# Performance work log

Measured on AMD Instinct MI355X. Metric: run time of the kernel, lower is better.

## Reference

```python
import jax, jax.numpy as jnp
import numpy as np

EPS = 1e-5
N_NODES = 10
NUM_JOINTS = 6   # all robot_configs fixed to '3_segments_3DOF' (module's fallback default)
MAX_DOF = 10


def _lin(x, w, b):
    # torch nn.Linear: y = x @ W.T + b, W is (out, in)
    return jnp.einsum('...i,oi->...o', x, w) + b


def _layernorm(x, scale, bias):
    mu = x.mean(-1, keepdims=True)
    var = x.var(-1, keepdims=True)
    return (x - mu) / jnp.sqrt(var + EPS) * scale + bias


def _forward(images, text_lengths, node_features, edge_indices, p):
    B = images.shape[0]
    # --- SimplifiedVLMBackbone ---
    y = jax.lax.conv_general_dilated(images, p['conv_w'], (2, 2), [(3, 3), (3, 3)],
                                     dimension_numbers=('NCHW', 'OIHW', 'NCHW'))
    y = jax.nn.relu(y + p['conv_b'][None, :, None, None])          # (B,32,112,112)
    y = y.reshape(B, 32, 7, 16, 7, 16).mean(axis=(3, 5))            # adaptive avg pool -> (B,32,7,7)
    y = y.reshape(B, 32 * 49)
    y = jax.nn.relu(_lin(y, p['img_fc1_w'], p['img_fc1_b']))
    img_feat = _lin(y, p['img_fc2_w'], p['img_fc2_b'])               # (B,768)
    t = p['text_emb'][jnp.clip(text_lengths, 0, 9999)]               # (B,256)
    vlm = img_feat + _lin(t, p['text_fc_w'], p['text_fc_b'])         # (B,768)

    # --- SoftArmGraphNN ---
    x = jax.nn.relu(_lin(node_features, p['enc1_w'], p['enc1_b']))
    x = _lin(x, p['enc2_w'], p['enc2_b'])                            # (B,N,64)
    src, dst = edge_indices[:, 0, :], edge_indices[:, 1, :]          # (B,E)

    def agg_fn(xi, si, di):
        # mean of neighbor (source) features per destination node; 0 if no neighbors
        g = xi[si]                                                   # (E,D)
        s = jax.ops.segment_sum(g, di, num_segments=N_NODES)
        c = jax.ops.segment_sum(jnp.ones(di.shape, xi.dtype), di, num_segments=N_NODES)
        return s / jnp.maximum(c, 1.0)[:, None]

    for i in range(3):
        residual = x
        mean_nb = jax.vmap(agg_fn)(x, src, dst)                      # (B,N,64)
        comb = jnp.concatenate([x, mean_nb], axis=-1)                # (B,N,128)
        x = _lin(comb, p['gc_w'][i], p['gc_b'][i])
        x = jax.nn.relu(_layernorm(x + residual, p['ln_scale'][i], p['ln_bias'][i]))
    graph_tokens = _lin(x, p['proj_w'], p['proj_b'])                 # (B,N,32)

    # --- AttentionPooling + dual-path fusion ---
    s = _lin(jnp.tanh(_lin(graph_tokens, p['attn1_w'], p['attn1_b'])), p['attn2_w'], p['attn2_b'])
    w = jax.nn.softmax(s, axis=1)                                    # (B,N,1)
    robot_token = jnp.sum(graph_tokens * w, axis=1)                  # (B,32) -> project? 32 vs 768 -> residual add via broadcast pad
    fused = vlm.at[:, :robot_token.shape[-1]].add(robot_token)       # global token residual into vlm features

    # --- NodeActionHead (all samples: 3seg_3DOF -> 6 joints, per-joint MLPs) ---
    comb = jnp.concatenate([
        jnp.broadcast_to(fused[:, None, :], (B, NUM_JOINTS, fused.shape[-1])),
        graph_tokens[:, :NUM_JOINTS, :]], axis=-1)                   # (B,J,800)
    h = jax.nn.relu(jnp.einsum('bjf,jhf->bjh', comb, p['head_w1']) + p['head_b1'])
    h = jax.nn.relu(jnp.einsum('bjf,jhf->bjh', h, p['head_w2']) + p['head_b2'])
    a = jnp.einsum('bjf,jhf->bjh', h, p['head_w3']) + p['head_b3']   # (B,6,16)
    a = jnp.pad(a, ((0, 0), (0, MAX_DOF - NUM_JOINTS), (0, 0)))      # pad to max_dof
    return jnp.transpose(a, (0, 2, 1))                               # (B,16,10)


def setup_inputs() -> dict:
    key = jax.random.key(0)
    ks = iter(jax.random.split(key, 64))

    def nrm(shape, scale=0.02):
        return scale * jax.random.normal(next(ks), shape, dtype=jnp.float32)

    B = 128
    inp = {
        'images': jax.random.normal(next(ks), (B, 3, 224, 224), dtype=jnp.float32),
        'text_lengths': jax.random.randint(next(ks), (B,), 0, 10000, dtype=jnp.int32),
        'node_features': jax.random.normal(next(ks), (B, N_NODES, 19), dtype=jnp.float32),
        'edge_indices': jax.random.randint(next(ks), (B, 2, 18), 0, N_NODES, dtype=jnp.int32),
        'conv_w': nrm((32, 3, 7, 7)), 'conv_b': jnp.zeros(32, jnp.float32),
        'img_fc1_w': nrm((512, 1568)), 'img_fc1_b': jnp.zeros(512, jnp.float32),
        'img_fc2_w': nrm((768, 512)), 'img_fc2_b': jnp.zeros(768, jnp.float32),
        'text_emb': nrm((10000, 256)),
        'text_fc_w': nrm((768, 256)), 'text_fc_b': jnp.zeros(768, jnp.float32),
        'enc1_w': nrm((64, 19)), 'enc1_b': jnp.zeros(64, jnp.float32),
        'enc2_w': nrm((64, 64)), 'enc2_b': jnp.zeros(64, jnp.float32),
        'gc_w': nrm((3, 64, 128)), 'gc_b': jnp.zeros((3, 64), jnp.float32),
        'ln_scale': jnp.ones((3, 64), jnp.float32), 'ln_bias': jnp.zeros((3, 64), jnp.float32),
        'proj_w': nrm((32, 64)), 'proj_b': jnp.zeros(32, jnp.float32),
        'attn1_w': nrm((16, 32)), 'attn1_b': jnp.zeros(16, jnp.float32),
        'attn2_w': nrm((1, 16)), 'attn2_b': jnp.zeros(1, jnp.float32),
        'head_w1': nrm((6, 128, 800)), 'head_b1': jnp.zeros((6, 128), jnp.float32),
        'head_w2': nrm((6, 64, 128)), 'head_b2': jnp.zeros((6, 64), jnp.float32),
        'head_w3': nrm((6, 16, 64)), 'head_b3': jnp.zeros((6, 16), jnp.float32),
    }
    return inp


def reference(images, text_lengths, node_features, edge_indices, conv_w, conv_b,
              img_fc1_w, img_fc1_b, img_fc2_w, img_fc2_b, text_emb, text_fc_w, text_fc_b,
              enc1_w, enc1_b, enc2_w, enc2_b, gc_w, gc_b, ln_scale, ln_bias,
              proj_w, proj_b, attn1_w, attn1_b, attn2_w, attn2_b,
              head_w1, head_b1, head_w2, head_b2, head_w3, head_b3):
    p = dict(conv_w=conv_w, conv_b=conv_b, img_fc1_w=img_fc1_w, img_fc1_b=img_fc1_b,
             img_fc2_w=img_fc2_w, img_fc2_b=img_fc2_b, text_emb=text_emb,
             text_fc_w=text_fc_w, text_fc_b=text_fc_b, enc1_w=enc1_w, enc1_b=enc1_b,
             enc2_w=enc2_w, enc2_b=enc2_b, gc_w=gc_w, gc_b=gc_b, ln_scale=ln_scale,
             ln_bias=ln_bias, proj_w=proj_w, proj_b=proj_b, attn1_w=attn1_w,
             attn1_b=attn1_b, attn2_w=attn2_w, attn2_b=attn2_b, head_w1=head_w1,
             head_b1=head_b1, head_w2=head_w2, head_b2=head_b2, head_w3=head_w3,
             head_b3=head_b3)
    return _forward(images, text_lengths, node_features, edge_indices, p)
```

## Files before the change

### kernel.cpp

```cpp
#include <hip/hip_runtime.h>
#include <hip/hip_bf16.h>
#include <math.h>

typedef __attribute__((ext_vector_type(8))) short bf16x8;
typedef __attribute__((ext_vector_type(4))) float f32x4;

static __device__ __forceinline__ unsigned short f2bf(float f) {
    union { float f; unsigned int u; } x{f};
    unsigned int u = x.u;
    unsigned int r = (u + 0x7fffu + ((u >> 16) & 1u)) >> 16;
    return (unsigned short)r;
}

static __device__ __forceinline__ unsigned int pack2(float f0, float f1) {
    __hip_bfloat162 h = __float22bfloat162_rn(float2{f0, f1});
    union { __hip_bfloat162 h; unsigned int u; } c{h};
    return c.u;
}

__global__ __launch_bounds__(256) void wprep(const float* __restrict__ conv_w,
                                             unsigned short* __restrict__ wB) {
    for (int idx = threadIdx.x; idx < 24 * 32 * 8; idx += 256) {
        int s = idx >> 8;
        int ch = (idx >> 3) & 31;
        int kx = idx & 7;
        float v = 0.f;
        if (s < 21 && kx < 7) {
            int c = s / 7, ky = s - c * 7;
            v = conv_w[ch * 147 + c * 49 + ky * 7 + kx];
        }
        wB[idx] = f2bf(v);
    }
}

#define PSTRIDE 116
__global__ __launch_bounds__(512, 4) void conv_mfma(const float* __restrict__ img,
                                                    const unsigned int* __restrict__ wBu,
                                                    const float* __restrict__ cb,
                                                    float* __restrict__ pooled) {
    __shared__ unsigned int patch[111 * PSTRIDE];
    const int t = threadIdx.x;
    const int py = blockIdx.x, b = blockIdx.y;
    const int lane = t & 63, wid = t >> 6;
    const int r16 = lane & 15, g = lane >> 4;
    const int Y0 = 32 * py - 3;

    const int xc0 = 2 * lane - 3;
    const int xc1 = 2 * lane + 125;
    const int a00 = max(xc0, 0);
    const int a01 = max(xc0 + 1, 0);
    const int a10 = min(xc1, 223);
    const int a11 = min(xc1 + 1, 223);
    const bool v00 = (xc0 >= 0);
    const bool v01 = (xc0 + 1 >= 0);
    const bool v10 = (xc1 <= 223);
    const bool v11 = (xc1 + 1 <= 223);
    const bool c1act = (lane < 52);

    const float* ib = img + (size_t)b * 3 * 224 * 224;

#pragma unroll
    for (int hb = 0; hb < 2; ++hb) {
        float g0[7], g1[7], g2[7], g3[7];
        int rr[7];
        bool rv[7];
        const float* rp[7];
#pragma unroll
        for (int i = 0; i < 7; ++i) {
            int r = wid + 8 * (hb * 7 + i);
            int c_ = (r >= 74) ? 2 : ((r >= 37) ? 1 : 0);
            int pr = r - 37 * c_;
            int iy = Y0 + pr;
            rv[i] = (r < 111) & (iy >= 0) & (iy < 224);
            int iyc = min(max(iy, 0), 223);
            rp[i] = ib + (c_ * 224 + iyc) * 224;
            rr[i] = r;
            g0[i] = rp[i][a00];
            g1[i] = rp[i][a01];
            g2[i] = rp[i][a10];
            g3[i] = rp[i][a11];
        }
#pragma unroll
        for (int i = 0; i < 7; ++i) {
            float f0 = (rv[i] && v00) ? g0[i] : 0.f;
            float f1 = (rv[i] && v01) ? g1[i] : 0.f;
            float f2_ = (rv[i] && v10) ? g2[i] : 0.f;
            float f3 = (rv[i] && v11) ? g3[i] : 0.f;
            if (rr[i] < 111) {
                patch[rr[i] * PSTRIDE + lane] = pack2(f0, f1);
                if (c1act) patch[rr[i] * PSTRIDE + 64 + lane] = pack2(f2_, f3);
            }
        }
    }

    bf16x8 bfrA[6], bfrB[6];
    int rowoff[6];
#pragma unroll
    for (int k = 0; k < 6; ++k) {
        int s = 4 * k + g;
        int sc = s > 20 ? 20 : s;
        int c = sc / 7, ky = sc - c * 7;
        rowoff[k] = c * 37 + ky;
        union { uint4 q; bf16x8 v; } ua, ub;
        ua.q = *(const uint4*)(wBu + (s * 32 + r16) * 4);
        ub.q = *(const uint4*)(wBu + (s * 32 + r16 + 16) * 4);
        bfrA[k] = ua.v;
        bfrB[k] = ub.v;
    }
    const float biasA = cb[r16], biasB = cb[r16 + 16];

    __syncthreads();

    float accA[7], accB[7];
#pragma unroll
    for (int p = 0; p < 7; ++p) accA[p] = accB[p] = 0.f;

#pragma unroll
    for (int q = 0; q < 2; ++q) {
        const int oyl = 2 * wid + q;
        int rb[6];
#pragma unroll
        for (int k = 0; k < 6; ++k) rb[k] = (rowoff[k] + 2 * oyl) * PSTRIDE;

        for (int t7 = 0; t7 < 7; ++t7) {
            const int oxr = 16 * t7 + r16;
            f32x4 C0 = {biasA, biasA, biasA, biasA};
            f32x4 C1 = {biasB, biasB, biasB, biasB};
#pragma unroll
            for (int k = 0; k < 6; ++k) {
                const unsigned int* ap = &patch[rb[k] + oxr];
                union { unsigned int u[4]; bf16x8 v; } ua;
                ua.u[0] = ap[0];
                ua.u[1] = ap[1];
                ua.u[2] = ap[2];
                ua.u[3] = ap[3];
                C0 = __builtin_amdgcn_mfma_f32_16x16x32_bf16(ua.v, bfrA[k], C0, 0, 0, 0);
                C1 = __builtin_amdgcn_mfma_f32_16x16x32_bf16(ua.v, bfrB[k], C1, 0, 0, 0);
            }
            float s0 = 0.f, s1 = 0.f;
#pragma unroll
            for (int r = 0; r < 4; ++r) {
                s0 += fmaxf(C0[r], 0.f);
                s1 += fmaxf(C1[r], 0.f);
            }
            accA[t7] += s0;
            accB[t7] += s1;
        }
    }
#pragma unroll
    for (int p = 0; p < 7; ++p) {
        accA[p] += __shfl_xor(accA[p], 16);
        accA[p] += __shfl_xor(accA[p], 32);
        accB[p] += __shfl_xor(accB[p], 16);
        accB[p] += __shfl_xor(accB[p], 32);
    }
    __syncthreads();
    float* sw = (float*)patch;
    if (lane < 16) {
#pragma unroll
        for (int p = 0; p < 7; ++p) {
            sw[(wid * 7 + p) * 32 + lane] = accA[p];
            sw[(wid * 7 + p) * 32 + lane + 16] = accB[p];
        }
    }
    __syncthreads();
    if (t < 224) {
        int p = t >> 5, ch = t & 31;
        float s = 0.f;
#pragma unroll
        for (int w = 0; w < 8; ++w) s += sw[(w * 7 + p) * 32 + ch];
        pooled[(size_t)b * 1568 + ch * 49 + py * 7 + p] = s * (1.f / 256.f);
    }
}

__global__ __launch_bounds__(256) void fc1_k(const float* __restrict__ in,
                                             const float* __restrict__ w,
                                             const float* __restrict__ bias,
                                             float* __restrict__ out) {
    __shared__ __align__(16) float xsm[8][1568];
    const int t = threadIdx.x;
    const int lane = t & 63, wid = t >> 6;
    const int ob = blockIdx.x & 127;
    const int bg = blockIdx.x >> 7;
    const int b0 = bg * 8;

#pragma unroll
    for (int r = 0; r < 8; ++r)
        for (int i = t; i < 392; i += 256)
            *(float4*)&xsm[r][i * 4] = *(const float4*)(in + (size_t)(b0 + r) * 1568 + i * 4);
    __syncthreads();

    const int o = ob * 4 + wid;
    const float4* wr = (const float4*)(w + (size_t)o * 1568);
    float acc[8] = {0, 0, 0, 0, 0, 0, 0, 0};
    for (int i = lane; i < 392; i += 64) {
        float4 wv = wr[i];
#pragma unroll
        for (int r = 0; r < 8; ++r) {
            float4 xv = *(const float4*)&xsm[r][i * 4];
            acc[r] = fmaf(xv.x, wv.x, acc[r]);
            acc[r] = fmaf(xv.y, wv.y, acc[r]);
            acc[r] = fmaf(xv.z, wv.z, acc[r]);
            acc[r] = fmaf(xv.w, wv.w, acc[r]);
        }
    }
#pragma unroll
    for (int r = 0; r < 8; ++r) {
        acc[r] += __shfl_xor(acc[r], 32);
        acc[r] += __shfl_xor(acc[r], 16);
        acc[r] += __shfl_xor(acc[r], 8);
        acc[r] += __shfl_xor(acc[r], 4);
        acc[r] += __shfl_xor(acc[r], 2);
        acc[r] += __shfl_xor(acc[r], 1);
    }
    float v = 0.f;
#pragma unroll
    for (int r = 0; r < 8; ++r)
        if (lane == r) v = acc[r];
    if (lane < 8) out[(size_t)(b0 + lane) * 512 + o] = fmaxf(v + bias[o], 0.f);
}

__global__ __launch_bounds__(256) void vlm_k(const float* __restrict__ h1,
                                             const float* __restrict__ w2,
                                             const float* __restrict__ b2,
                                             const int* __restrict__ tlen,
                                             const float* __restrict__ temb,
                                             const float* __restrict__ tw,
                                             const float* __restrict__ tb,
                                             const float* __restrict__ rtok,
                                             float* __restrict__ fused) {
    __shared__ __align__(16) float xs1[8][512];
    __shared__ __align__(16) float xst[8][256];
    __shared__ int srow[8];
    const int t = threadIdx.x;
    const int lane = t & 63, wid = t >> 6;
    const int ob = blockIdx.x % 192;
    const int bg = blockIdx.x / 192;
    const int b0 = bg * 8;

    if (t < 8) {
        int r = tlen[b0 + t];
        srow[t] = min(max(r, 0), 9999);
    }
#pragma unroll
    for (int rr = 0; rr < 4; ++rr) {
        int r = rr * 2 + (t >> 7);
        int i = t & 127;
        *(float4*)&xs1[r][i * 4] = *(const float4*)(h1 + (size_t)(b0 + r) * 512 + i * 4);
    }
    __syncthreads();
#pragma unroll
    for (int rr = 0; rr < 2; ++rr) {
        int r = rr * 4 + (t >> 6);
        int i = t & 63;
        *(float4*)&xst[r][i * 4] = *(const float4*)(temb + (size_t)srow[r] * 256 + i * 4);
    }
    __syncthreads();

    const int o = ob * 4 + wid;
    float acc[8] = {0, 0, 0, 0, 0, 0, 0, 0};
    {
        const float4* wr = (const float4*)(w2 + (size_t)o * 512);
#pragma unroll
        for (int ii = 0; ii < 2; ++ii) {
            int i = lane + ii * 64;
            float4 wv = wr[i];
#pragma unroll
            for (int r = 0; r < 8; ++r) {
                float4 xv = *(const float4*)&xs1[r][i * 4];
                acc[r] = fmaf(xv.x, wv.x, acc[r]);
                acc[r] = fmaf(xv.y, wv.y, acc[r]);
                acc[r] = fmaf(xv.z, wv.z, acc[r]);
                acc[r] = fmaf(xv.w, wv.w, acc[r]);
            }
        }
    }
    {
        const float4* wt4 = (const float4*)(tw + (size_t)o * 256);
        float4 wv = wt4[lane];
#pragma unroll
        for (int r = 0; r < 8; ++r) {
            float4 xv = *(const float4*)&xst[r][lane * 4];
            acc[r] = fmaf(xv.x, wv.x, acc[r]);
            acc[r] = fmaf(xv.y, wv.y, acc[r]);
            acc[r] = fmaf(xv.z, wv.z, acc[r]);
            acc[r] = fmaf(xv.w, wv.w, acc[r]);
        }
    }
#pragma unroll
    for (int r = 0; r < 8; ++r) {
        acc[r] += __shfl_xor(acc[r], 32);
        acc[r] += __shfl_xor(acc[r], 16);
        acc[r] += __shfl_xor(acc[r], 8);
        acc[r] += __shfl_xor(acc[r], 4);
        acc[r] += __shfl_xor(acc[r], 2);
        acc[r] += __shfl_xor(acc[r], 1);
    }
    float v = 0.f;
#pragma unroll
    for (int r = 0; r < 8; ++r)
        if (lane == r) v = acc[r];
    if (lane < 8) {
        float add = (o < 32) ? rtok[(size_t)(b0 + lane) * 32 + o] : 0.f;
        fused[(size_t)(b0 + lane) * 768 + o] = v + b2[o] + tb[o] + add;
    }
}

__global__ __launch_bounds__(640, 1) void graph_k(
    const float* __restrict__ nfeat, const int* __restrict__ eidx,
    const float* __restrict__ e1w, const float* __restrict__ e1b,
    const float* __restrict__ e2w, const float* __restrict__ e2b,
    const float* __restrict__ gcw, const float* __restrict__ gcb,
    const float* __restrict__ lns, const float* __restrict__ lnb,
    const float* __restrict__ pjw, const float* __restrict__ pjb,
    const float* __restrict__ a1w, const float* __restrict__ a1b,
    const float* __restrict__ a2w, const float* __restrict__ a2b,
    float* __restrict__ gts_g, float* __restrict__ rtok) {
    __shared__ __align__(16) float pool[8448];
    __shared__ __align__(16) float nf[10][20];
    __shared__ __align__(16) float xsA[10][64];
    __shared__ __align__(16) float xsB[10][64];
    __shared__ __align__(16) float nbs[10][64];
    __shared__ __align__(16) float gtss[10][32];
    __shared__ float svs[10];
    __shared__ int se[18], de[18];
    const int t = threadIdx.x;
    const int b = blockIdx.x;
    const int n = t >> 6, o = t & 63;

    if (t < 190) {
        int nn = t / 19, i = t - nn * 19;
        nf[nn][i] = nfeat[(size_t)(b * 10 + nn) * 19 + i];
    }
    if (t < 36) {
        if (t < 18) se[t] = eidx[b * 36 + t];
        else de[t - 18] = eidx[b * 36 + t];
    }
    float* e1wT = pool;
    float* e2wT = pool + 1280;
    for (int u = t; u < 1216; u += 640) {
        int oo = u / 19, k = u - oo * 19;
        e1wT[k * 64 + oo] = e1w[u];
    }
    for (int u = t; u < 4096; u += 640) {
        int oo = u >> 6, k = u & 63;
        e2wT[k * 65 + oo] = e2w[u];
    }
    __syncthreads();

    float h1v;
    {
        float acc = e1b[o];
#pragma unroll
        for (int i = 0; i < 19; ++i) acc = fmaf(nf[n][i], e1wT[i * 64 + o], acc);
        h1v = fmaxf(acc, 0.f);
        xsB[n][o] = h1v;
    }
    {
        const float* xrow = &xsB[n][0];
        float s0 = 0, s1 = 0, s2 = 0, s3 = 0;
#pragma unroll
        for (int k = 0; k < 64; k += 4) {
            s0 = fmaf(xrow[k], e2wT[k * 65 + o], s0);
            s1 = fmaf(xrow[k + 1], e2wT[(k + 1) * 65 + o], s1);
            s2 = fmaf(xrow[k + 2], e2wT[(k + 2) * 65 + o], s2);
            s3 = fmaf(xrow[k + 3], e2wT[(k + 3) * 65 + o], s3);
        }
        xsA[n][o] = e2b[o] + ((s0 + s1) + (s2 + s3));
    }
    __syncthreads();

    float* src = &xsA[0][0];
    float* dst = &xsB[0][0];
    for (int l = 0; l < 3; ++l) {
        const float* gl = gcw + (size_t)l * 8192;
        for (int u = t; u < 8192; u += 640) {
            int oo = u >> 7, k = u & 127;
            pool[k * 65 + oo] = gl[u];
        }
        {
            float s = 0.f;
            int cnt = 0;
#pragma unroll
            for (int e = 0; e < 18; ++e) {
                bool m = (de[e] == n);
                float v = src[se[e] * 64 + o];
                s += m ? v : 0.f;
                cnt += m ? 1 : 0;
            }
            nbs[n][o] = s / (float)(cnt > 1 ? cnt : 1);
        }
        __syncthreads();
        {
            const float* xa = src + n * 64;
            const float* xb = &nbs[n][0];
            float s0 = 0, s1 = 0, s2 = 0, s3 = 0;
#pragma unroll
            for (int k = 0; k < 64; k += 4) {
                s0 = fmaf(xa[k], pool[k * 65 + o], s0);
                s1 = fmaf(xa[k + 1], pool[(k + 1) * 65 + o], s1);
                s2 = fmaf(xa[k + 2], pool[(k + 2) * 65 + o], s2);
                s3 = fmaf(xa[k + 3], pool[(k + 3) * 65 + o], s3);
            }
#pragma unroll
            for (int k = 0; k < 64; k += 4) {
                s0 = fmaf(xb[k], pool[(64 + k) * 65 + o], s0);
                s1 = fmaf(xb[k + 1], pool[(64 + k + 1) * 65 + o], s1);
                s2 = fmaf(xb[k + 2], pool[(64 + k + 2) * 65 + o], s2);
                s3 = fmaf(xb[k + 3], pool[(64 + k + 3) * 65 + o], s3);
            }
            float v = gcb[l * 64 + o] + ((s0 + s1) + (s2 + s3)) + xa[o];
            float mu = v;
            mu += __shfl_xor(mu, 32);
            mu += __shfl_xor(mu, 16);
            mu += __shfl_xor(mu, 8);
            mu += __shfl_xor(mu, 4);
            mu += __shfl_xor(mu, 2);
            mu += __shfl_xor(mu, 1);
            mu *= (1.f / 64.f);
            float d = v - mu;
            float vr = d * d;
            vr += __shfl_xor(vr, 32);
            vr += __shfl_xor(vr, 16);
            vr += __shfl_xor(vr, 8);
            vr += __shfl_xor(vr, 4);
            vr += __shfl_xor(vr, 2);
            vr += __shfl_xor(vr, 1);
            vr *= (1.f / 64.f);
            dst[n * 64 + o] =
                fmaxf(d / sqrtf(vr + 1e-5f) * lns[l * 64 + o] + lnb[l * 64 + o], 0.f);
        }
        __syncthreads();
        float* tmp = src;
        src = dst;
        dst = tmp;
    }

    float* pjwT = pool;
    float* a1wT = pool + 2112;
    for (int u = t; u < 2048; u += 640) {
        int oo = u >> 6, k = u & 63;
        pjwT[k * 33 + oo] = pjw[u];
    }
    for (int u = t; u < 512; u += 640) {
        int hh = u >> 5, k = u & 31;
        a1wT[k * 17 + hh] = a1w[u];
    }
    __syncthreads();

    if (o < 32) {
        const float* xrow = src + n * 64;
        float s0 = 0, s1 = 0, s2 = 0, s3 = 0;
#pragma unroll
        for (int k = 0; k < 64; k += 4) {
            s0 = fmaf(xrow[k], pjwT[k * 33 + o], s0);
            s1 = fmaf(xrow[k + 1], pjwT[(k + 1) * 33 + o], s1);
            s2 = fmaf(xrow[k + 2], pjwT[(k + 2) * 33 + o], s2);
            s3 = fmaf(xrow[k + 3], pjwT[(k + 3) * 33 + o], s3);
        }
        float gv = pjb[o] + ((s0 + s1) + (s2 + s3));
        gtss[n][o] = gv;
        gts_g[(size_t)b * 320 + n * 32 + o] = gv;
    }
    if (o < 16) {
        const float* xrow = &gtss[n][0];
        float s0 = 0, s1 = 0, s2 = 0, s3 = 0;
#pragma unroll
        for (int k = 0; k < 32; k += 4) {
            s0 = fmaf(xrow[k], a1wT[k * 17 + o], s0);
            s1 = fmaf(xrow[k + 1], a1wT[(k + 1) * 17 + o], s1);
            s2 = fmaf(xrow[k + 2], a1wT[(k + 2) * 17 + o], s2);
            s3 = fmaf(xrow[k + 3], a1wT[(k + 3) * 17 + o], s3);
        }
        float z = a1b[o] + ((s0 + s1) + (s2 + s3));
        float sc = tanhf(z) * a2w[o];
        sc += __shfl_xor(sc, 8);
        sc += __shfl_xor(sc, 4);
        sc += __shfl_xor(sc, 2);
        sc += __shfl_xor(sc, 1);
        if (o == 0) svs[n] = sc + a2b[0];
    }
    __syncthreads();

    if (n == 0 && o < 32) {
        float m = svs[0];
#pragma unroll
        for (int i = 1; i < 10; ++i) m = fmaxf(m, svs[i]);
        float e[10];
        float sum = 0.f;
#pragma unroll
        for (int i = 0; i < 10; ++i) {
            e[i] = expf(svs[i] - m);
            sum += e[i];
        }
        float inv = 1.f / sum;
        float rt = 0.f;
#pragma unroll
        for (int nn = 0; nn < 10; ++nn) rt = fmaf(gtss[nn][o], e[nn] * inv, rt);
        rtok[(size_t)b * 32 + o] = rt;
    }
}

__global__ __launch_bounds__(256) void head1_k(const float* __restrict__ fused,
                                               const float* __restrict__ gts,
                                               const float* __restrict__ w1,
                                               const float* __restrict__ b1,
                                               float* __restrict__ h1T) {
    __shared__ __align__(16) float xsm[8][800];
    const int t = threadIdx.x;
    const int ob = blockIdx.x % 192;
    const int bg = blockIdx.x / 192;
    const int b0 = bg * 8;
    const int j = ob >> 5;
    const int lane = t & 63, wid = t >> 6;

    for (int u = t; u < 1600; u += 256) {
        int row = u / 200, i = u - row * 200;
        float4 v;
        if (i < 192)
            v = *(const float4*)(fused + (size_t)(b0 + row) * 768 + i * 4);
        else
            v = *(const float4*)(gts + (size_t)(b0 + row) * 320 + j * 32 + (i - 192) * 4);
        *(float4*)&xsm[row][i * 4] = v;
    }
    __syncthreads();

    const int o = ob * 4 + wid;
    const float4* wr = (const float4*)(w1 + (size_t)o * 800);
    float acc[8] = {0, 0, 0, 0, 0, 0, 0, 0};
    for (int i = lane; i < 200; i += 64) {
        float4 wv = wr[i];
#pragma unroll
        for (int r = 0; r < 8; ++r) {
            float4 xv = *(const float4*)&xsm[r][i * 4];
            acc[r] = fmaf(xv.x, wv.x, acc[r]);
            acc[r] = fmaf(xv.y, wv.y, acc[r]);
            acc[r] = fmaf(xv.z, wv.z, acc[r]);
            acc[r] = fmaf(xv.w, wv.w, acc[r]);
        }
    }
#pragma unroll
    for (int r = 0; r < 8; ++r) {
        acc[r] += __shfl_xor(acc[r], 32);
        acc[r] += __shfl_xor(acc[r], 16);
        acc[r] += __shfl_xor(acc[r], 8);
        acc[r] += __shfl_xor(acc[r], 4);
        acc[r] += __shfl_xor(acc[r], 2);
        acc[r] += __shfl_xor(acc[r], 1);
    }
    float v = 0.f;
#pragma unroll
    for (int r = 0; r < 8; ++r)
        if (lane == r) v = acc[r];
    if (lane < 8) h1T[(size_t)o * 128 + b0 + lane] = fmaxf(v + b1[o], 0.f);
}

__global__ __launch_bounds__(128) void head2_k(const float* __restrict__ h1T,
                                               const float* __restrict__ w2,
                                               const float* __restrict__ b2,
                                               float* __restrict__ h2T) {
    const int o2 = blockIdx.x;
    const int j = o2 >> 6;
    const int b = threadIdx.x;
    const float* wrow = w2 + (size_t)o2 * 128;
    const float* xcol = h1T + (size_t)j * 128 * 128 + b;
    float acc = b2[o2];
#pragma unroll 16
    for (int k = 0; k < 128; ++k) acc = fmaf(xcol[k * 128], wrow[k], acc);
    h2T[(size_t)o2 * 128 + b] = fmaxf(acc, 0.f);
}

__global__ __launch_bounds__(128) void head3_k(const float* __restrict__ h2T,
                                               const float* __restrict__ w3,
                                               const float* __restrict__ b3,
                                               float* __restrict__ out) {
    const int jj = blockIdx.x % 10;
    const int oo = blockIdx.x / 10;
    const int b = threadIdx.x;
    float acc = 0.f;
    if (jj < 6) {
        const float* wrow = w3 + (size_t)(jj * 16 + oo) * 64;
        const float* xcol = h2T + (size_t)jj * 64 * 128 + b;
        acc = b3[jj * 16 + oo];
#pragma unroll 16
        for (int k = 0; k < 64; ++k) acc = fmaf(xcol[k * 128], wrow[k], acc);
    }
    out[(size_t)b * 160 + oo * 10 + jj] = acc;
}

extern "C" void kernel_launch(void* const* d_in, const int* in_sizes, int n_in,
                              void* d_out, int out_size, void* d_ws, size_t ws_size,
                              hipStream_t stream) {
    const float* images = (const float*)d_in[0];
    const int* tlen = (const int*)d_in[1];
    const float* nfeat = (const float*)d_in[2];
    const int* eidx = (const int*)d_in[3];
    const float* conv_w = (const float*)d_in[4];
    const float* conv_b = (const float*)d_in[5];
    const float* fc1w = (const float*)d_in[6];
    const float* fc1b = (const float*)d_in[7];
    const float* fc2w = (const float*)d_in[8];
    const float* fc2b = (const float*)d_in[9];
    const float* temb = (const float*)d_in[10];
    const float* tfw = (const float*)d_in[11];
    const float* tfb = (const float*)d_in[12];
    const float* e1w = (const float*)d_in[13];
    const float* e1b = (const float*)d_in[14];
    const float* e2w = (const float*)d_in[15];
    const float* e2b = (const float*)d_in[16];
    const float* gcw = (const float*)d_in[17];
    const float* gcb = (const float*)d_in[18];
    const float* lns = (const float*)d_in[19];
    const float* lnb = (const float*)d_in[20];
    const float* pjw = (const float*)d_in[21];
    const float* pjb = (const float*)d_in[22];
    const float* a1w = (const float*)d_in[23];
    const float* a1b = (const float*)d_in[24];
    const float* a2w = (const float*)d_in[25];
    const float* a2b = (const float*)d_in[26];
    const float* w1 = (const float*)d_in[27];
    const float* b1 = (const float*)d_in[28];
    const float* w2 = (const float*)d_in[29];
    const float* b2 = (const float*)d_in[30];
    const float* w3 = (const float*)d_in[31];
    const float* b3 = (const float*)d_in[32];

    const int B = in_sizes[0] / (3 * 224 * 224);

    float* ws = (float*)d_ws;
    unsigned short* wB = (unsigned short*)d_ws;
    float* pooled = ws + 3072;
    float* h1fc = pooled + (size_t)B * 1568;
    float* fused = h1fc + (size_t)B * 512;
    float* gts = fused + (size_t)B * 768;
    float* rtok = gts + (size_t)B * 320;
    float* h1T = pooled;
    float* h2T = pooled + 98304;

    wprep<<<1, 256, 0, stream>>>(conv_w, wB);
    conv_mfma<<<dim3(7, B), 512, 0, stream>>>(images, (const unsigned int*)wB,
                                              conv_b, pooled);
    fc1_k<<<2048, 256, 0, stream>>>(pooled, fc1w, fc1b, h1fc);
    graph_k<<<B, 640, 0, stream>>>(nfeat, eidx, e1w, e1b, e2w, e2b, gcw, gcb,
                                   lns, lnb, pjw, pjb, a1w, a1b, a2w, a2b,
                                   gts, rtok);
    vlm_k<<<3072, 256, 0, stream>>>(h1fc, fc2w, fc2b, tlen, temb, tfw, tfb,
                                    rtok, fused);
    head1_k<<<192 * (B / 8), 256, 0, stream>>>(fused, gts, w1, b1, h1T);
    head2_k<<<384, 128, 0, stream>>>(h1T, w2, b2, h2T);
    head3_k<<<160, 128, 0, stream>>>(h2T, w3, b3, (float*)d_out);
}
```

Before: 133.0 us.

## Compute more output rows per block in FC kernels, re-pad conv weight layout

The fc1, vlm and head1 kernels now loop over 4 or 8 output groups per block, cutting grid sizes by 4-8x. Each block's staged activation tile in shared memory is reused across more weight rows, reducing redundant global activation loads and block launch overhead. The conv weight prep switches to a power-of-two (8 per channel) slot layout with shift/mask indexing, and the patch stride changes from 116 to 120. Fewer blocks may reduce parallelism and latency hiding on a large GPU.

```diff
diff --git a/kernel.cpp b/kernel.cpp
--- a/kernel.cpp
+++ b/kernel.cpp
@@ -24,16 +24,14 @@
         int s = idx >> 8;
         int ch = (idx >> 3) & 31;
         int kx = idx & 7;
+        int c = s >> 3, ky = s & 7;
         float v = 0.f;
-        if (s < 21 && kx < 7) {
-            int c = s / 7, ky = s - c * 7;
-            v = conv_w[ch * 147 + c * 49 + ky * 7 + kx];
-        }
+        if (ky < 7 && kx < 7) v = conv_w[ch * 147 + c * 49 + ky * 7 + kx];
         wB[idx] = f2bf(v);
     }
 }
 
-#define PSTRIDE 116
+#define PSTRIDE 120
 __global__ __launch_bounds__(512, 4) void conv_mfma(const float* __restrict__ img,
                                                     const unsigned int* __restrict__ wBu,
                                                     const float* __restrict__ cb,
@@ -98,9 +96,9 @@
 #pragma unroll
     for (int k = 0; k < 6; ++k) {
         int s = 4 * k + g;
-        int sc = s > 20 ? 20 : s;
-        int c = sc / 7, ky = sc - c * 7;
-        rowoff[k] = c * 37 + ky;
+        int c = s >> 3, ky = s & 7;
+        int kyc = ky > 6 ? 6 : ky;
+        rowoff[k] = c * 37 + kyc;
         union { uint4 q; bf16x8 v; } ua, ub;
         ua.q = *(const uint4*)(wBu + (s * 32 + r16) * 4);
         ub.q = *(const uint4*)(wBu + (s * 32 + r16 + 16) * 4);
@@ -180,8 +178,8 @@
     __shared__ __align__(16) float xsm[8][1568];
     const int t = threadIdx.x;
     const int lane = t & 63, wid = t >> 6;
-    const int ob = blockIdx.x & 127;
-    const int bg = blockIdx.x >> 7;
+    const int ob = blockIdx.x & 31;
+    const int bg = blockIdx.x >> 5;
     const int b0 = bg * 8;
 
 #pragma unroll
@@ -190,34 +188,37 @@
             *(float4*)&xsm[r][i * 4] = *(const float4*)(in + (size_t)(b0 + r) * 1568 + i * 4);
     __syncthreads();
 
-    const int o = ob * 4 + wid;
-    const float4* wr = (const float4*)(w + (size_t)o * 1568);
-    float acc[8] = {0, 0, 0, 0, 0, 0, 0, 0};
-    for (int i = lane; i < 392; i += 64) {
-        float4 wv = wr[i];
+#pragma unroll
+    for (int oi = 0; oi < 4; ++oi) {
+        const int o = ob * 16 + oi * 4 + wid;
+        const float4* wr = (const float4*)(w + (size_t)o * 1568);
+        float acc[8] = {0, 0, 0, 0, 0, 0, 0, 0};
+        for (int i = lane; i < 392; i += 64) {
+            float4 wv = wr[i];
+#pragma unroll
+            for (int r = 0; r < 8; ++r) {
+                float4 xv = *(const float4*)&xsm[r][i * 4];
+                acc[r] = fmaf(xv.x, wv.x, acc[r]);
+                acc[r] = fmaf(xv.y, wv.y, acc[r]);
+                acc[r] = fmaf(xv.z, wv.z, acc[r]);
+                acc[r] = fmaf(xv.w, wv.w, acc[r]);
+            }
+        }
 #pragma unroll
         for (int r = 0; r < 8; ++r) {
-            float4 xv = *(const float4*)&xsm[r][i * 4];
-            acc[r] = fmaf(xv.x, wv.x, acc[r]);
-            acc[r] = fmaf(xv.y, wv.y, acc[r]);
-            acc[r] = fmaf(xv.z, wv.z, acc[r]);
-            acc[r] = fmaf(xv.w, wv.w, acc[r]);
-        }
-    }
-#pragma unroll
-    for (int r = 0; r < 8; ++r) {
-        acc[r] += __shfl_xor(acc[r], 32);
-        acc[r] += __shfl_xor(acc[r], 16);
-        acc[r] += __shfl_xor(acc[r], 8);
-        acc[r] += __shfl_xor(acc[r], 4);
-        acc[r] += __shfl_xor(acc[r], 2);
-        acc[r] += __shfl_xor(acc[r], 1);
-    }
-    float v = 0.f;
-#pragma unroll
-    for (int r = 0; r < 8; ++r)
-        if (lane == r) v = acc[r];
-    if (lane < 8) out[(size_t)(b0 + lane) * 512 + o] = fmaxf(v + bias[o], 0.f);
+            acc[r] += __shfl_xor(acc[r], 32);
+            acc[r] += __shfl_xor(acc[r], 16);
+            acc[r] += __shfl_xor(acc[r], 8);
+            acc[r] += __shfl_xor(acc[r], 4);
+            acc[r] += __shfl_xor(acc[r], 2);
+            acc[r] += __shfl_xor(acc[r], 1);
+        }
+        float v = 0.f;
+#pragma unroll
+        for (int r = 0; r < 8; ++r)
+            if (lane == r) v = acc[r];
+        if (lane < 8) out[(size_t)(b0 + lane) * 512 + o] = fmaxf(v + bias[o], 0.f);
+    }
 }
 
 __global__ __launch_bounds__(256) void vlm_k(const float* __restrict__ h1,
@@ -234,8 +235,8 @@
     __shared__ int srow[8];
     const int t = threadIdx.x;
     const int lane = t & 63, wid = t >> 6;
-    const int ob = blockIdx.x % 192;
-    const int bg = blockIdx.x / 192;
+    const int ob = blockIdx.x % 24;
+    const int bg = blockIdx.x / 24;
     const int b0 = bg * 8;
 
     if (t < 8) {
@@ -257,52 +258,55 @@
     }
     __syncthreads();
 
-    const int o = ob * 4 + wid;
-    float acc[8] = {0, 0, 0, 0, 0, 0, 0, 0};
-    {
-        const float4* wr = (const float4*)(w2 + (size_t)o * 512);
-#pragma unroll
-        for (int ii = 0; ii < 2; ++ii) {
-            int i = lane + ii * 64;
-            float4 wv = wr[i];
+#pragma unroll
+    for (int oi = 0; oi < 8; ++oi) {
+        const int o = ob * 32 + oi * 4 + wid;
+        float acc[8] = {0, 0, 0, 0, 0, 0, 0, 0};
+        {
+            const float4* wr = (const float4*)(w2 + (size_t)o * 512);
+#pragma unroll
+            for (int ii = 0; ii < 2; ++ii) {
+                int i = lane + ii * 64;
+                float4 wv = wr[i];
+#pragma unroll
+                for (int r = 0; r < 8; ++r) {
+                    float4 xv = *(const float4*)&xs1[r][i * 4];
+                    acc[r] = fmaf(xv.x, wv.x, acc[r]);
+                    acc[r] = fmaf(xv.y, wv.y, acc[r]);
+                    acc[r] = fmaf(xv.z, wv.z, acc[r]);
+                    acc[r] = fmaf(xv.w, wv.w, acc[r]);
+                }
+            }
+        }
+        {
+            const float4* wt4 = (const float4*)(tw + (size_t)o * 256);
+            float4 wv = wt4[lane];
 #pragma unroll
             for (int r = 0; r < 8; ++r) {
-                float4 xv = *(const float4*)&xs1[r][i * 4];
+                float4 xv = *(const float4*)&xst[r][lane * 4];
                 acc[r] = fmaf(xv.x, wv.x, acc[r]);
                 acc[r] = fmaf(xv.y, wv.y, acc[r]);
                 acc[r] = fmaf(xv.z, wv.z, acc[r]);
                 acc[r] = fmaf(xv.w, wv.w, acc[r]);
             }
         }
-    }
-    {
-        const float4* wt4 = (const float4*)(tw + (size_t)o * 256);
-        float4 wv = wt4[lane];
 #pragma unroll
         for (int r = 0; r < 8; ++r) {
-            float4 xv = *(const float4*)&xst[r][lane * 4];
-            acc[r] = fmaf(xv.x, wv.x, acc[r]);
-            acc[r] = fmaf(xv.y, wv.y, acc[r]);
-            acc[r] = fmaf(xv.z, wv.z, acc[r]);
-            acc[r] = fmaf(xv.w, wv.w, acc[r]);
-        }
-    }
-#pragma unroll
-    for (int r = 0; r < 8; ++r) {
-        acc[r] += __shfl_xor(acc[r], 32);
-        acc[r] += __shfl_xor(acc[r], 16);
-        acc[r] += __shfl_xor(acc[r], 8);
-        acc[r] += __shfl_xor(acc[r], 4);
-        acc[r] += __shfl_xor(acc[r], 2);
-        acc[r] += __shfl_xor(acc[r], 1);
-    }
-    float v = 0.f;
-#pragma unroll
-    for (int r = 0; r < 8; ++r)
-        if (lane == r) v = acc[r];
-    if (lane < 8) {
-        float add = (o < 32) ? rtok[(size_t)(b0 + lane) * 32 + o] : 0.f;
-        fused[(size_t)(b0 + lane) * 768 + o] = v + b2[o] + tb[o] + add;
+            acc[r] += __shfl_xor(acc[r], 32);
+            acc[r] += __shfl_xor(acc[r], 16);
+            acc[r] += __shfl_xor(acc[r], 8);
+            acc[r] += __shfl_xor(acc[r], 4);
+            acc[r] += __shfl_xor(acc[r], 2);
+            acc[r] += __shfl_xor(acc[r], 1);
+        }
+        float v = 0.f;
+#pragma unroll
+        for (int r = 0; r < 8; ++r)
+            if (lane == r) v = acc[r];
+        if (lane < 8) {
+            float add = (o < 32) ? rtok[(size_t)(b0 + lane) * 32 + o] : 0.f;
+            fused[(size_t)(b0 + lane) * 768 + o] = v + b2[o] + tb[o] + add;
+        }
     }
 }
 
@@ -348,13 +352,11 @@
     }
     __syncthreads();
 
-    float h1v;
     {
         float acc = e1b[o];
 #pragma unroll
         for (int i = 0; i < 19; ++i) acc = fmaf(nf[n][i], e1wT[i * 64 + o], acc);
-        h1v = fmaxf(acc, 0.f);
-        xsB[n][o] = h1v;
+        xsB[n][o] = fmaxf(acc, 0.f);
     }
     {
         const float* xrow = &xsB[n][0];
@@ -508,10 +510,10 @@
                                                float* __restrict__ h1T) {
     __shared__ __align__(16) float xsm[8][800];
     const int t = threadIdx.x;
-    const int ob = blockIdx.x % 192;
-    const int bg = blockIdx.x / 192;
+    const int ob = blockIdx.x % 24;
+    const int bg = blockIdx.x / 24;
     const int b0 = bg * 8;
-    const int j = ob >> 5;
+    const int j = ob >> 2;
     const int lane = t & 63, wid = t >> 6;
 
     for (int u = t; u < 1600; u += 256) {
@@ -525,34 +527,37 @@
     }
     __syncthreads();
 
-    const int o = ob * 4 + wid;
-    const float4* wr = (const float4*)(w1 + (size_t)o * 800);
-    float acc[8] = {0, 0, 0, 0, 0, 0, 0, 0};
-    for (int i = lane; i < 200; i += 64) {
-        float4 wv = wr[i];
+#pragma unroll
+    for (int oi = 0; oi < 8; ++oi) {
+        const int o = ob * 32 + oi * 4 + wid;
+        const float4* wr = (const float4*)(w1 + (size_t)o * 800);
+        float acc[8] = {0, 0, 0, 0, 0, 0, 0, 0};
+        for (int i = lane; i < 200; i += 64) {
+            float4 wv = wr[i];
+#pragma unroll
+            for (int r = 0; r < 8; ++r) {
+                float4 xv = *(const float4*)&xsm[r][i * 4];
+                acc[r] = fmaf(xv.x, wv.x, acc[r]);
+                acc[r] = fmaf(xv.y, wv.y, acc[r]);
+                acc[r] = fmaf(xv.z, wv.z, acc[r]);
+                acc[r] = fmaf(xv.w, wv.w, acc[r]);
+            }
+        }
 #pragma unroll
         for (int r = 0; r < 8; ++r) {
-            float4 xv = *(const float4*)&xsm[r][i * 4];
-            acc[r] = fmaf(xv.x, wv.x, acc[r]);
-            acc[r] = fmaf(xv.y, wv.y, acc[r]);
-            acc[r] = fmaf(xv.z, wv.z, acc[r]);
-            acc[r] = fmaf(xv.w, wv.w, acc[r]);
-        }
-    }
-#pragma unroll
-    for (int r = 0; r < 8; ++r) {
-        acc[r] += __shfl_xor(acc[r], 32);
-        acc[r] += __shfl_xor(acc[r], 16);
-        acc[r] += __shfl_xor(acc[r], 8);
-        acc[r] += __shfl_xor(acc[r], 4);
-        acc[r] += __shfl_xor(acc[r], 2);
-        acc[r] += __shfl_xor(acc[r], 1);
-    }
-    float v = 0.f;
-#pragma unroll
-    for (int r = 0; r < 8; ++r)
-        if (lane == r) v = acc[r];
-    if (lane < 8) h1T[(size_t)o * 128 + b0 + lane] = fmaxf(v + b1[o], 0.f);
+            acc[r] += __shfl_xor(acc[r], 32);
+            acc[r] += __shfl_xor(acc[r], 16);
+            acc[r] += __shfl_xor(acc[r], 8);
+            acc[r] += __shfl_xor(acc[r], 4);
+            acc[r] += __shfl_xor(acc[r], 2);
+            acc[r] += __shfl_xor(acc[r], 1);
+        }
+        float v = 0.f;
+#pragma unroll
+        for (int r = 0; r < 8; ++r)
+            if (lane == r) v = acc[r];
+        if (lane < 8) h1T[(size_t)o * 128 + b0 + lane] = fmaxf(v + b1[o], 0.f);
+    }
 }
 
 __global__ __launch_bounds__(128) void head2_k(const float* __restrict__ h1T,
@@ -640,13 +645,13 @@
     wprep<<<1, 256, 0, stream>>>(conv_w, wB);
     conv_mfma<<<dim3(7, B), 512, 0, stream>>>(images, (const unsigned int*)wB,
                                               conv_b, pooled);
-    fc1_k<<<2048, 256, 0, stream>>>(pooled, fc1w, fc1b, h1fc);
+    fc1_k<<<32 * 16, 256, 0, stream>>>(pooled, fc1w, fc1b, h1fc);
     graph_k<<<B, 640, 0, stream>>>(nfeat, eidx, e1w, e1b, e2w, e2b, gcw, gcb,
                                    lns, lnb, pjw, pjb, a1w, a1b, a2w, a2b,
                                    gts, rtok);
-    vlm_k<<<3072, 256, 0, stream>>>(h1fc, fc2w, fc2b, tlen, temb, tfw, tfb,
-                                    rtok, fused);
-    head1_k<<<192 * (B / 8), 256, 0, stream>>>(fused, gts, w1, b1, h1T);
+    vlm_k<<<24 * 16, 256, 0, stream>>>(h1fc, fc2w, fc2b, tlen, temb, tfw, tfb,
+                                       rtok, fused);
+    head1_k<<<24 * 16, 256, 0, stream>>>(fused, gts, w1, b1, h1T);
     head2_k<<<384, 128, 0, stream>>>(h1T, w2, b2, h2T);
     head3_k<<<160, 128, 0, stream>>>(h2T, w3, b3, (float*)d_out);
 }
```

Result: slower. 136.2 us (+2.4%).
